# Kernel tuning notes

Measured on AMD Instinct MI355X. Metric: run time of the kernel, lower is better.

Reference implementation:

```python
import jax, jax.numpy as jnp
import numpy as np

N = 50000
E = 800000
IN_DIM = 128
HIDDEN = 96
HEADS = 4
HEAD_DIM = HIDDEN // HEADS
NUM_LAYERS = 3
NEG_SLOPE = 0.2


def _gat_layer(h, W, a_l, a_r, b, src, dst):
    # h: [N, F_in], W: [F_in, H*D], a_l/a_r: [H, D], b: [H, D]
    feat = (h @ W).reshape(N, HEADS, HEAD_DIM)          # [N, H, D]
    el = jnp.sum(feat * a_l, axis=-1)                    # [N, H]
    er = jnp.sum(feat * a_r, axis=-1)                    # [N, H]
    e = el[src] + er[dst]                                # [E, H]
    e = jnp.where(e > 0, e, NEG_SLOPE * e)               # leaky_relu
    # edge softmax over incoming edges of each dst node
    m = jax.ops.segment_max(e, dst, num_segments=N)      # [N, H]
    ex = jnp.exp(e - m[dst])                             # [E, H]
    denom = jax.ops.segment_sum(ex, dst, num_segments=N) # [N, H]
    alpha = ex / denom[dst]                              # [E, H]
    msg = feat[src] * alpha[:, :, None]                  # [E, H, D]
    out = jax.ops.segment_sum(msg, dst, num_segments=N)  # [N, H, D]
    out = out + b                                        # bias
    out = jax.nn.elu(out)                                # activation
    return out.reshape(N, HEADS * HEAD_DIM)              # flatten(1)


def setup_inputs() -> dict:
    key = jax.random.key(0)
    ks = jax.random.split(key, 16)
    feats = jax.random.normal(ks[0], (N, IN_DIM), dtype=jnp.float32)
    src = jax.random.randint(ks[1], (E,), 0, N)
    dst = jax.random.randint(ks[2], (E,), 0, N)
    inp = {"feats": feats, "src": src, "dst": dst}
    fin = IN_DIM
    for l in range(NUM_LAYERS):
        s = 1.0 / np.sqrt(fin)
        inp[f"W{l}"] = jax.random.normal(ks[3 + 4 * l], (fin, HIDDEN), dtype=jnp.float32) * s
        inp[f"al{l}"] = jax.random.normal(ks[4 + 4 * l], (HEADS, HEAD_DIM), dtype=jnp.float32) * 0.1
        inp[f"ar{l}"] = jax.random.normal(ks[5 + 4 * l], (HEADS, HEAD_DIM), dtype=jnp.float32) * 0.1
        inp[f"b{l}"] = jnp.zeros((HEADS, HEAD_DIM), dtype=jnp.float32)
        fin = HIDDEN
    return inp


def reference(feats, src, dst, W0, al0, ar0, b0, W1, al1, ar1, b1, W2, al2, ar2, b2):
    h = feats
    params = [(W0, al0, ar0, b0), (W1, al1, ar1, b1), (W2, al2, ar2, b2)]
    for (W, al, ar, b) in params:
        h = _gat_layer(h, W, al, ar, b, src, dst)
    # AvgPooling over all nodes (single graph) -> [1, HIDDEN]
    return jnp.mean(h, axis=0, keepdims=True)
```

## Files before the change

kernel.cpp:

```cpp
#include <hip/hip_runtime.h>
#include <hip/hip_bf16.h>

#define N_NODES 50000
#define E_EDGES 800000
#define IN_DIM  128
#define HIDDEN  96
#define HEADS   4
#define HEAD_DIM 24
#define NEG_SLOPE 0.2f


__global__ void k_hist(const int* __restrict__ dst, int* __restrict__ deg) {
    int e = blockIdx.x * 256 + threadIdx.x;
    if (e < E_EDGES) atomicAdd(&deg[dst[e]], 1);
}

__global__ __launch_bounds__(256) void k_scan1(const int* __restrict__ deg,
                                               int* __restrict__ bsum, int n) {
    int i = blockIdx.x * 256 + threadIdx.x;
    int v = (i < n) ? deg[i] : 0;
#pragma unroll
    for (int s = 1; s < 64; s <<= 1) v += __shfl_xor(v, s);
    __shared__ int ws[4];
    if ((threadIdx.x & 63) == 0) ws[threadIdx.x >> 6] = v;
    __syncthreads();
    if (threadIdx.x == 0) bsum[blockIdx.x] = ws[0] + ws[1] + ws[2] + ws[3];
}

__global__ __launch_bounds__(256) void k_scan2(int* __restrict__ bsum, int nb) {
    int tid = threadIdx.x;
    int v = (tid < nb) ? bsum[tid] : 0;
    int lane = tid & 63, wv = tid >> 6;
    int x = v;
#pragma unroll
    for (int s = 1; s < 64; s <<= 1) {
        int t = __shfl_up(x, s);
        if (lane >= s) x += t;
    }
    __shared__ int wsum[4];
    if (lane == 63) wsum[wv] = x;
    __syncthreads();
    int add = 0;
    for (int w = 0; w < wv; ++w) add += wsum[w];
    x += add;
    if (tid < nb) bsum[tid] = x - v;
}

__global__ __launch_bounds__(256) void k_scan3(const int* __restrict__ deg,
                                               const int* __restrict__ bsum,
                                               int* __restrict__ off, int n) {
    int tid = threadIdx.x;
    int i = blockIdx.x * 256 + tid;
    int v = (i < n) ? deg[i] : 0;
    int lane = tid & 63, wv = tid >> 6;
    int x = v;
#pragma unroll
    for (int s = 1; s < 64; s <<= 1) {
        int t = __shfl_up(x, s);
        if (lane >= s) x += t;
    }
    __shared__ int wsum[4];
    if (lane == 63) wsum[wv] = x;
    __syncthreads();
    int add = bsum[blockIdx.x];
    for (int w = 0; w < wv; ++w) add += wsum[w];
    if (i < n) off[i] = x - v + add;
    if (i == n - 1) off[n] = x + add;
}

__global__ void k_fill(const int* __restrict__ src, const int* __restrict__ dst,
                       const int* __restrict__ off, int* __restrict__ cursor,
                       int* __restrict__ ssrc) {
    int e = blockIdx.x * 256 + threadIdx.x;
    if (e < E_EDGES) {
        int d = dst[e];
        int p = off[d] + atomicAdd(&cursor[d], 1);
        ssrc[p] = src[e];
    }
}


template <int K>
__global__ __launch_bounds__(384) void k_gemm(const float* __restrict__ h,
                                              const float* __restrict__ W,
                                              float* __restrict__ feat, int n) {
    __shared__ float hl[64 * K];
    int node0 = blockIdx.x * 64;
    int total4 = 64 * K / 4;
    for (int idx = threadIdx.x; idx < total4; idx += 384) {
        int node = idx / (K / 4);
        int koff = (idx % (K / 4)) * 4;
        float4 v = make_float4(0.f, 0.f, 0.f, 0.f);
        if (node0 + node < n)
            v = *(const float4*)(&h[(size_t)(node0 + node) * K + koff]);
        *(float4*)(&hl[node * K + koff]) = v;
    }
    __syncthreads();
    int grp = threadIdx.x / 48;
    int c = (threadIdx.x % 48) * 2;
    int nb = grp * 8;
    float acc[8][2];
#pragma unroll
    for (int i = 0; i < 8; ++i) acc[i][0] = acc[i][1] = 0.f;
    for (int k = 0; k < K; k += 4) {
        float2 w0 = *(const float2*)&W[(k + 0) * 96 + c];
        float2 w1 = *(const float2*)&W[(k + 1) * 96 + c];
        float2 w2 = *(const float2*)&W[(k + 2) * 96 + c];
        float2 w3 = *(const float2*)&W[(k + 3) * 96 + c];
#pragma unroll
        for (int i = 0; i < 8; ++i) {
            float4 hv = *(const float4*)&hl[(nb + i) * K + k];
            acc[i][0] = fmaf(hv.x, w0.x, acc[i][0]);
            acc[i][1] = fmaf(hv.x, w0.y, acc[i][1]);
            acc[i][0] = fmaf(hv.y, w1.x, acc[i][0]);
            acc[i][1] = fmaf(hv.y, w1.y, acc[i][1]);
            acc[i][0] = fmaf(hv.z, w2.x, acc[i][0]);
            acc[i][1] = fmaf(hv.z, w2.y, acc[i][1]);
            acc[i][0] = fmaf(hv.w, w3.x, acc[i][0]);
            acc[i][1] = fmaf(hv.w, w3.y, acc[i][1]);
        }
    }
#pragma unroll
    for (int i = 0; i < 8; ++i) {
        int node = node0 + nb + i;
        if (node < n) *(float2*)&feat[(size_t)node * 96 + c] = make_float2(acc[i][0], acc[i][1]);
    }
}

__global__ void k_elr(const float* __restrict__ feat, const float* __restrict__ al,
                      const float* __restrict__ ar, float* __restrict__ el,
                      float* __restrict__ er, int n) {
    int idx = blockIdx.x * blockDim.x + threadIdx.x;
    if (idx >= n * 4) return;
    int node = idx >> 2, h = idx & 3;
    const float* f = &feat[(size_t)node * 96 + h * 24];
    const float* alh = &al[h * 24];
    const float* arh = &ar[h * 24];
    float sl = 0.f, sr = 0.f;
#pragma unroll
    for (int d4 = 0; d4 < 6; ++d4) {
        float4 v = *(const float4*)&f[d4 * 4];
        float4 a = *(const float4*)&alh[d4 * 4];
        float4 b = *(const float4*)&arh[d4 * 4];
        sl = fmaf(v.x, a.x, sl); sl = fmaf(v.y, a.y, sl);
        sl = fmaf(v.z, a.z, sl); sl = fmaf(v.w, a.w, sl);
        sr = fmaf(v.x, b.x, sr); sr = fmaf(v.y, b.y, sr);
        sr = fmaf(v.z, b.z, sr); sr = fmaf(v.w, b.w, sr);
    }
    el[idx] = sl;
    er[idx] = sr;
}

__global__ __launch_bounds__(256) void k_agg(const int* __restrict__ off,
                                             const int* __restrict__ ssrc,
                                             const float* __restrict__ el,
                                             const float* __restrict__ er,
                                             const float* __restrict__ feat,
                                             const float* __restrict__ bias,
                                             float* __restrict__ out) {
    int n = blockIdx.x * 4 + (threadIdx.x >> 6);
    if (n >= N_NODES) return;
    int lane = threadIdx.x & 63;
    int j0   = lane >> 3;
    int h    = (lane >> 1) & 3;
    int half = lane & 1;
    int cbase = h * 24 + half * 12;

    int start = off[n], deg = off[n + 1] - start;
    float er_h = er[n * 4 + h];

    float e_reg[4];
    int   s_reg[4];
    float lmax = -1e30f;
#pragma unroll
    for (int t = 0; t < 4; ++t) {
        int j = t * 8 + j0;
        bool act = (j < deg);
        int s = act ? ssrc[start + j] : 0;
        float e = -1e30f;
        if (act) {
            e = el[s * 4 + h] + er_h;
            e = (e > 0.f) ? e : NEG_SLOPE * e;
        }
        s_reg[t] = s;
        e_reg[t] = e;
        lmax = fmaxf(lmax, e);
    }
    for (int j = 32 + j0; j < deg; j += 8) {
        int s = ssrc[start + j];
        float e = el[s * 4 + h] + er_h;
        e = (e > 0.f) ? e : NEG_SLOPE * e;
        lmax = fmaxf(lmax, e);
    }
    lmax = fmaxf(lmax, __shfl_xor(lmax, 8));
    lmax = fmaxf(lmax, __shfl_xor(lmax, 16));
    lmax = fmaxf(lmax, __shfl_xor(lmax, 32));
    float m = lmax;

    float acc[12];
#pragma unroll
    for (int c = 0; c < 12; ++c) acc[c] = 0.f;
    float den = 0.f;
#pragma unroll
    for (int t = 0; t < 4; ++t) {
        int j = t * 8 + j0;
        if (j < deg) {
            float ex = expf(e_reg[t] - m);
            den += ex;
            const float* fr = &feat[(size_t)s_reg[t] * 96 + cbase];
            float4 v0 = *(const float4*)(fr + 0);
            float4 v1 = *(const float4*)(fr + 4);
            float4 v2 = *(const float4*)(fr + 8);
            acc[0] = fmaf(ex, v0.x, acc[0]);  acc[1] = fmaf(ex, v0.y, acc[1]);
            acc[2] = fmaf(ex, v0.z, acc[2]);  acc[3] = fmaf(ex, v0.w, acc[3]);
            acc[4] = fmaf(ex, v1.x, acc[4]);  acc[5] = fmaf(ex, v1.y, acc[5]);
            acc[6] = fmaf(ex, v1.z, acc[6]);  acc[7] = fmaf(ex, v1.w, acc[7]);
            acc[8] = fmaf(ex, v2.x, acc[8]);  acc[9] = fmaf(ex, v2.y, acc[9]);
            acc[10] = fmaf(ex, v2.z, acc[10]); acc[11] = fmaf(ex, v2.w, acc[11]);
        }
    }
    for (int j = 32 + j0; j < deg; j += 8) {
        int s = ssrc[start + j];
        float e = el[s * 4 + h] + er_h;
        e = (e > 0.f) ? e : NEG_SLOPE * e;
        float ex = expf(e - m);
        den += ex;
        const float* fr = &feat[(size_t)s * 96 + cbase];
        float4 v0 = *(const float4*)(fr + 0);
        float4 v1 = *(const float4*)(fr + 4);
        float4 v2 = *(const float4*)(fr + 8);
        acc[0] = fmaf(ex, v0.x, acc[0]);  acc[1] = fmaf(ex, v0.y, acc[1]);
        acc[2] = fmaf(ex, v0.z, acc[2]);  acc[3] = fmaf(ex, v0.w, acc[3]);
        acc[4] = fmaf(ex, v1.x, acc[4]);  acc[5] = fmaf(ex, v1.y, acc[5]);
        acc[6] = fmaf(ex, v1.z, acc[6]);  acc[7] = fmaf(ex, v1.w, acc[7]);
        acc[8] = fmaf(ex, v2.x, acc[8]);  acc[9] = fmaf(ex, v2.y, acc[9]);
        acc[10] = fmaf(ex, v2.z, acc[10]); acc[11] = fmaf(ex, v2.w, acc[11]);
    }

#pragma unroll
    for (int st = 8; st <= 32; st <<= 1) {
        den += __shfl_xor(den, st);
#pragma unroll
        for (int c = 0; c < 12; ++c) acc[c] += __shfl_xor(acc[c], st);
    }

    if (j0 == 0) {
        float rden = (den > 0.f) ? 1.f / den : 0.f;
        const float* bp = &bias[cbase];
        float o[12];
#pragma unroll
        for (int c = 0; c < 12; ++c) {
            float v = acc[c] * rden + bp[c];
            o[c] = (v > 0.f) ? v : (expf(v) - 1.f);
        }
        float* op = &out[(size_t)n * 96 + cbase];
        *(float4*)(op + 0) = make_float4(o[0], o[1], o[2], o[3]);
        *(float4*)(op + 4) = make_float4(o[4], o[5], o[6], o[7]);
        *(float4*)(op + 8) = make_float4(o[8], o[9], o[10], o[11]);
    }
}

__global__ __launch_bounds__(128) void k_pool(const float* __restrict__ h,
                                              float* __restrict__ out) {
    int tid = threadIdx.x;
    if (tid >= 96) return;
    float a = 0.f;
    for (int nrow = blockIdx.x; nrow < N_NODES; nrow += gridDim.x)
        a += h[(size_t)nrow * 96 + tid];
    atomicAdd(&out[tid], a * (1.0f / N_NODES));
}


extern "C" void kernel_launch(void* const* d_in, const int* in_sizes, int n_in,
                              void* d_out, int out_size, void* d_ws, size_t ws_size,
                              hipStream_t stream) {
    const float* feats = (const float*)d_in[0];
    const int* src = (const int*)d_in[1];
    const int* dst = (const int*)d_in[2];

    char* p = (char*)d_ws;
    auto alloc = [&](size_t bytes) {
        void* r = (void*)p;
        p += (bytes + 255) & ~(size_t)255;
        return r;
    };
    float* A      = (float*)alloc((size_t)N_NODES * 96 * 4);
    float* B      = (float*)alloc((size_t)N_NODES * 96 * 4);
    float* el     = (float*)alloc((size_t)N_NODES * 4 * 4);
    float* er     = (float*)alloc((size_t)N_NODES * 4 * 4);
    int* degcur   = (int*)alloc((size_t)N_NODES * 2 * 4);
    int* off      = (int*)alloc((size_t)(N_NODES + 1) * 4);
    int* bsum     = (int*)alloc((size_t)256 * 4);
    int* ssrc     = (int*)alloc((size_t)E_EDGES * 4);
    int* deg = degcur;
    int* cursor = degcur + N_NODES;

    hipMemsetAsync(degcur, 0, (size_t)N_NODES * 2 * 4, stream);
    hipMemsetAsync(d_out, 0, (size_t)out_size * 4, stream);

    const int NB = (N_NODES + 255) / 256;
    k_hist<<<(E_EDGES + 255) / 256, 256, 0, stream>>>(dst, deg);
    k_scan1<<<NB, 256, 0, stream>>>(deg, bsum, N_NODES);
    k_scan2<<<1, 256, 0, stream>>>(bsum, NB);
    k_scan3<<<NB, 256, 0, stream>>>(deg, bsum, off, N_NODES);
    k_fill<<<(E_EDGES + 255) / 256, 256, 0, stream>>>(src, dst, off, cursor, ssrc);

    const float* hin = feats;
    for (int l = 0; l < 3; ++l) {
        const float* W  = (const float*)d_in[3 + 4 * l];
        const float* al = (const float*)d_in[4 + 4 * l];
        const float* ar = (const float*)d_in[5 + 4 * l];
        const float* bb = (const float*)d_in[6 + 4 * l];

        if (l == 0)
            k_gemm<IN_DIM><<<(N_NODES + 63) / 64, 384, 0, stream>>>(hin, W, B, N_NODES);
        else
            k_gemm<HIDDEN><<<(N_NODES + 63) / 64, 384, 0, stream>>>(hin, W, B, N_NODES);

        k_elr<<<(N_NODES * 4 + 255) / 256, 256, 0, stream>>>(B, al, ar, el, er, N_NODES);
        k_agg<<<(N_NODES + 3) / 4, 256, 0, stream>>>(off, ssrc, el, er, B, bb, A);
        hin = A;
    }

    k_pool<<<256, 128, 0, stream>>>(A, (float*)d_out);
}
```

Before: 485.9 us.

## Fuse attention logit computation into GEMM epilogue and use two-stage pooling

The per-node el/er attention dot products are now computed inside the GEMM epilogue via a shared-memory partial reduction, which removes the separate k_elr kernel and its re-read of the feature matrix in every layer. Mean pooling is split into a block-partial pass and a single-block final reduction, replacing the float atomics and the output memset. The fused epilogue adds two block barriers and extra shared memory, which may lower GEMM occupancy.

```diff
diff --git a/kernel.cpp b/kernel.cpp
--- a/kernel.cpp
+++ b/kernel.cpp
@@ -8,6 +8,7 @@
 #define HEADS   4
 #define HEAD_DIM 24
 #define NEG_SLOPE 0.2f
+#define POOL_BLOCKS 256
 
 
 __global__ void k_hist(const int* __restrict__ dst, int* __restrict__ deg) {
@@ -83,8 +84,17 @@
 template <int K>
 __global__ __launch_bounds__(384) void k_gemm(const float* __restrict__ h,
                                               const float* __restrict__ W,
-                                              float* __restrict__ feat, int n) {
-    __shared__ float hl[64 * K];
+                                              const float* __restrict__ al_g,
+                                              const float* __restrict__ ar_g,
+                                              float* __restrict__ feat,
+                                              float* __restrict__ el,
+                                              float* __restrict__ er, int n) {
+    constexpr int HL = 64 * K;
+    constexpr int PT = 384 * 17;
+    constexpr int SM = (HL > PT) ? HL : PT;
+    __shared__ float smem[SM];
+    float* hl = smem;
+
     int node0 = blockIdx.x * 64;
     int total4 = 64 * K / 4;
     for (int idx = threadIdx.x; idx < total4; idx += 384) {
@@ -125,30 +135,34 @@
         int node = node0 + nb + i;
         if (node < n) *(float2*)&feat[(size_t)node * 96 + c] = make_float2(acc[i][0], acc[i][1]);
     }
-}
-
-__global__ void k_elr(const float* __restrict__ feat, const float* __restrict__ al,
-                      const float* __restrict__ ar, float* __restrict__ el,
-                      float* __restrict__ er, int n) {
-    int idx = blockIdx.x * blockDim.x + threadIdx.x;
-    if (idx >= n * 4) return;
-    int node = idx >> 2, h = idx & 3;
-    const float* f = &feat[(size_t)node * 96 + h * 24];
-    const float* alh = &al[h * 24];
-    const float* arh = &ar[h * 24];
-    float sl = 0.f, sr = 0.f;
-#pragma unroll
-    for (int d4 = 0; d4 < 6; ++d4) {
-        float4 v = *(const float4*)&f[d4 * 4];
-        float4 a = *(const float4*)&alh[d4 * 4];
-        float4 b = *(const float4*)&arh[d4 * 4];
-        sl = fmaf(v.x, a.x, sl); sl = fmaf(v.y, a.y, sl);
-        sl = fmaf(v.z, a.z, sl); sl = fmaf(v.w, a.w, sl);
-        sr = fmaf(v.x, b.x, sr); sr = fmaf(v.y, b.y, sr);
-        sr = fmaf(v.z, b.z, sr); sr = fmaf(v.w, b.w, sr);
-    }
-    el[idx] = sl;
-    er[idx] = sr;
+    float alc0 = al_g[c], alc1 = al_g[c + 1];
+    float arc0 = ar_g[c], arc1 = ar_g[c + 1];
+    __syncthreads();
+    float* part = smem;
+    int base = threadIdx.x * 17;
+#pragma unroll
+    for (int i = 0; i < 8; ++i) {
+        part[base + i * 2]     = acc[i][0] * alc0 + acc[i][1] * alc1;
+        part[base + i * 2 + 1] = acc[i][0] * arc0 + acc[i][1] * arc1;
+    }
+    __syncthreads();
+    if (threadIdx.x < 256) {
+        int ig = threadIdx.x >> 2;
+        int hh = threadIdx.x & 3;
+        int g2 = ig >> 3, il = ig & 7;
+        float se = 0.f, sr = 0.f;
+#pragma unroll
+        for (int cc = 0; cc < 12; ++cc) {
+            int t = g2 * 48 + hh * 12 + cc;
+            se += part[t * 17 + il * 2];
+            sr += part[t * 17 + il * 2 + 1];
+        }
+        int node = node0 + ig;
+        if (node < n) {
+            el[node * 4 + hh] = se;
+            er[node * 4 + hh] = sr;
+        }
+    }
 }
 
 __global__ __launch_bounds__(256) void k_agg(const int* __restrict__ off,
@@ -260,14 +274,32 @@
     }
 }
 
-__global__ __launch_bounds__(128) void k_pool(const float* __restrict__ h,
-                                              float* __restrict__ out) {
-    int tid = threadIdx.x;
-    if (tid >= 96) return;
+__global__ __launch_bounds__(384) void k_pool1(const float* __restrict__ h,
+                                               float* __restrict__ partial) {
+    int r = threadIdx.x / 96;
+    int c = threadIdx.x % 96;
     float a = 0.f;
-    for (int nrow = blockIdx.x; nrow < N_NODES; nrow += gridDim.x)
-        a += h[(size_t)nrow * 96 + tid];
-    atomicAdd(&out[tid], a * (1.0f / N_NODES));
+    for (int nrow = blockIdx.x * 4 + r; nrow < N_NODES; nrow += POOL_BLOCKS * 4)
+        a += h[(size_t)nrow * 96 + c];
+    __shared__ float sred[4][96];
+    sred[r][c] = a;
+    __syncthreads();
+    if (r == 0)
+        partial[blockIdx.x * 96 + c] = sred[0][c] + sred[1][c] + sred[2][c] + sred[3][c];
+}
+
+__global__ __launch_bounds__(384) void k_pool2(const float* __restrict__ partial,
+                                               float* __restrict__ out) {
+    int g = threadIdx.x / 96;
+    int c = threadIdx.x % 96;
+    float a = 0.f;
+    for (int b = g; b < POOL_BLOCKS; b += 4)
+        a += partial[b * 96 + c];
+    __shared__ float sred[4][96];
+    sred[g][c] = a;
+    __syncthreads();
+    if (g == 0)
+        out[c] = (sred[0][c] + sred[1][c] + sred[2][c] + sred[3][c]) * (1.0f / N_NODES);
 }
 
 
@@ -284,19 +316,19 @@
         p += (bytes + 255) & ~(size_t)255;
         return r;
     };
-    float* A      = (float*)alloc((size_t)N_NODES * 96 * 4);
-    float* B      = (float*)alloc((size_t)N_NODES * 96 * 4);
-    float* el     = (float*)alloc((size_t)N_NODES * 4 * 4);
-    float* er     = (float*)alloc((size_t)N_NODES * 4 * 4);
-    int* degcur   = (int*)alloc((size_t)N_NODES * 2 * 4);
-    int* off      = (int*)alloc((size_t)(N_NODES + 1) * 4);
-    int* bsum     = (int*)alloc((size_t)256 * 4);
-    int* ssrc     = (int*)alloc((size_t)E_EDGES * 4);
+    float* A       = (float*)alloc((size_t)N_NODES * 96 * 4);
+    float* B       = (float*)alloc((size_t)N_NODES * 96 * 4);
+    float* el      = (float*)alloc((size_t)N_NODES * 4 * 4);
+    float* er      = (float*)alloc((size_t)N_NODES * 4 * 4);
+    int* degcur    = (int*)alloc((size_t)N_NODES * 2 * 4);
+    int* off       = (int*)alloc((size_t)(N_NODES + 1) * 4);
+    int* bsum      = (int*)alloc((size_t)256 * 4);
+    int* ssrc      = (int*)alloc((size_t)E_EDGES * 4);
+    float* partial = (float*)alloc((size_t)POOL_BLOCKS * 96 * 4);
     int* deg = degcur;
     int* cursor = degcur + N_NODES;
 
     hipMemsetAsync(degcur, 0, (size_t)N_NODES * 2 * 4, stream);
-    hipMemsetAsync(d_out, 0, (size_t)out_size * 4, stream);
 
     const int NB = (N_NODES + 255) / 256;
     k_hist<<<(E_EDGES + 255) / 256, 256, 0, stream>>>(dst, deg);
@@ -313,14 +345,14 @@
         const float* bb = (const float*)d_in[6 + 4 * l];
 
         if (l == 0)
-            k_gemm<IN_DIM><<<(N_NODES + 63) / 64, 384, 0, stream>>>(hin, W, B, N_NODES);
+            k_gemm<IN_DIM><<<(N_NODES + 63) / 64, 384, 0, stream>>>(hin, W, al, ar, B, el, er, N_NODES);
         else
-            k_gemm<HIDDEN><<<(N_NODES + 63) / 64, 384, 0, stream>>>(hin, W, B, N_NODES);
-
-        k_elr<<<(N_NODES * 4 + 255) / 256, 256, 0, stream>>>(B, al, ar, el, er, N_NODES);
+            k_gemm<HIDDEN><<<(N_NODES + 63) / 64, 384, 0, stream>>>(hin, W, al, ar, B, el, er, N_NODES);
+
         k_agg<<<(N_NODES + 3) / 4, 256, 0, stream>>>(off, ssrc, el, er, B, bb, A);
         hin = A;
     }
 
-    k_pool<<<256, 128, 0, stream>>>(A, (float*)d_out);
-}
+    k_pool1<<<POOL_BLOCKS, 384, 0, stream>>>(A, partial);
+    k_pool2<<<1, 384, 0, stream>>>(partial, (float*)d_out);
+}
```

New measurement: 440.0 us. 1.1x faster.
